# Kernel tuning notes

Hardware: AMD Instinct MI355X
Metric: run time of the kernel (lower is better)

Reference implementation:

```python
import jax, jax.numpy as jnp
import numpy as np

B, C, H, W = 2, 192, 128, 128
DG, K = 4, 9  # deformable groups, kernel taps (3x3)


def conv3x3(x, w, b):
    y = jax.lax.conv_general_dilated(x, w, (1, 1), ((1, 1), (1, 1)),
                                     dimension_numbers=('NCHW', 'OIHW', 'NCHW'))
    return y + b[None, :, None, None]


def deform_sample(x, dy, dx, mask):
    # x: [B,C,H,W]; dy,dx,mask: [B,DG,K,H,W]. Returns [B,C,K,H,W] masked bilinear samples.
    b, c, h, w = x.shape
    cg = c // DG
    kk = jnp.arange(K)
    ky = (kk // 3 - 1).astype(x.dtype)  # kernel row offsets {-1,0,1}, pad=1, stride=1
    kx = (kk % 3 - 1).astype(x.dtype)
    ii = jnp.arange(h, dtype=x.dtype)
    jj = jnp.arange(w, dtype=x.dtype)
    py = ii[None, None, None, :, None] + ky[None, None, :, None, None] + dy  # [B,DG,K,H,W]
    px = jj[None, None, None, None, :] + kx[None, None, :, None, None] + dx
    y0 = jnp.floor(py)
    x0 = jnp.floor(px)
    ly = py - y0
    lx = px - x0
    xf = x.reshape(b, DG, cg, h * w)
    out = jnp.zeros((b, DG, cg, K, h, w), dtype=x.dtype)
    corners = [(y0, x0, (1 - ly) * (1 - lx)), (y0, x0 + 1, (1 - ly) * lx),
               (y0 + 1, x0, ly * (1 - lx)), (y0 + 1, x0 + 1, ly * lx)]
    for yc, xc, wt in corners:
        valid = (yc >= 0) & (yc < h) & (xc >= 0) & (xc < w)  # zero padding outside
        wv = wt * valid.astype(x.dtype)
        idx = (jnp.clip(yc, 0, h - 1) * w + jnp.clip(xc, 0, w - 1)).astype(jnp.int32)
        idxb = jnp.broadcast_to(idx.reshape(b, DG, 1, K * h * w), (b, DG, cg, K * h * w))
        g = jnp.take_along_axis(xf, idxb, axis=3).reshape(b, DG, cg, K, h, w)
        out = out + wv[:, :, None] * g
    out = out * mask[:, :, None]
    return out.reshape(b, c, K, h, w)


def setup_inputs() -> dict:
    key = jax.random.key(0)
    ks = jax.random.split(key, 8)
    f32 = jnp.float32
    x_vq = jax.random.normal(ks[0], (B, C, H, W), f32)
    x_residual = jax.random.normal(ks[1], (B, C, H, W), f32)
    w_off = jax.random.normal(ks[2], (C, 2 * C, 3, 3), f32) * (1.0 / np.sqrt(2 * C * 9))
    b_off = jnp.zeros((C,), f32)
    # conv_offset of DCNv2Pack: C -> 3*DG*K channels; small init keeps offsets moderate
    w_co = jax.random.normal(ks[3], (3 * DG * K, C, 3, 3), f32) * 0.02
    b_co = jnp.zeros((3 * DG * K,), f32)
    w_dcn = jax.random.normal(ks[4], (C, C, 3, 3), f32) * (1.0 / np.sqrt(C * 9))
    b_dcn = jnp.zeros((C,), f32)
    return {"x_vq": x_vq, "x_residual": x_residual, "w_off": w_off, "b_off": b_off,
            "w_co": w_co, "b_co": b_co, "w_dcn": w_dcn, "b_dcn": b_dcn}


def reference(x_vq, x_residual, w_off, b_off, w_co, b_co, w_dcn, b_dcn):
    feat = conv3x3(jnp.concatenate([x_vq, x_residual], axis=1), w_off, b_off)  # [B,C,H,W]
    off_out = conv3x3(feat, w_co, b_co)  # [B,3*DG*K,H,W]
    gk = DG * K
    o1 = off_out[:, :gk]
    o2 = off_out[:, gk:2 * gk]
    mask = jax.nn.sigmoid(off_out[:, 2 * gk:])
    dy = o1.reshape(B, DG, K, H, W)
    dx = o2.reshape(B, DG, K, H, W)
    m = mask.reshape(B, DG, K, H, W)
    sampled = deform_sample(x_vq, dy, dx, m)  # [B,C,K,H,W]
    y = jnp.einsum('ock,bckhw->bohw', w_dcn.reshape(C, C, K), sampled)
    return y + b_dcn[None, :, None, None]
```

## Files before the change

kernel.cpp:

```cpp
#include <hip/hip_runtime.h>
#include <math.h>

#define HH 128
#define WW 128
#define HW 16384
#define BB 2
#define CC 192

typedef __attribute__((ext_vector_type(8)))  short short8;
typedef __attribute__((ext_vector_type(4)))  float f32x4;
typedef __attribute__((ext_vector_type(16))) float f32x16;

static __device__ __forceinline__ short f2bf(float f) {
    unsigned u = __float_as_uint(f);
    unsigned r = (u + 0x7FFFu + ((u >> 16) & 1u)) >> 16;
    return (short)r;
}
static __device__ __forceinline__ float bf2f(short s) {
    return __uint_as_float(((unsigned)(unsigned short)s) << 16);
}

static __device__ __forceinline__ void gl_lds16(const short* gsrc, short* ldst) {
    __builtin_amdgcn_global_load_lds(
        (const __attribute__((address_space(1))) unsigned*)gsrc,
        (__attribute__((address_space(3))) unsigned*)ldst, 16, 0, 0);
}

__global__ __launch_bounds__(256) void to_grp_k(
    const float* __restrict__ xv, const float* __restrict__ xr,
    unsigned short* __restrict__ xg)
{
    const int idx = blockIdx.x * 256 + threadIdx.x;
    const int pos = idx & (HW - 1);
    const int cgb = idx >> 14;
    const int cg  = cgb % 48;
    const int b   = cgb / 48;
    short8 v;
#pragma unroll
    for (int r = 0; r < 8; r++) {
        const int c = cg * 8 + r;
        const float f = (c < 192)
            ? xv[((size_t)(b * 192 + c) << 14) + pos]
            : xr[((size_t)(b * 192 + (c - 192)) << 14) + pos];
        v[r] = f2bf(f);
    }
    *reinterpret_cast<short8*>(xg + (size_t)idx * 8) = v;
}

__global__ void pack_w_k(const float* __restrict__ w, short* __restrict__ wp,
                         int Co, int so, int d1, int s1, int d2, int s2, int s3,
                         int total)
{
    const int idx = blockIdx.x * blockDim.x + threadIdx.x;
    if (idx >= total) return;
    const int lane  = idx & 63;
    const int slot  = (idx >> 6) & 7;
    const int chunk = idx >> 9;
    const int o     = slot * 32 + (lane & 31);
    const int k0    = chunk * 16 + ((lane >> 5) << 3);
    short8 v;
#pragma unroll
    for (int r = 0; r < 8; r++) {
        const int k = k0 + r;
        float f = 0.f;
        if (o < Co) {
            const int rem = k % d1;
            f = w[(size_t)o * so + (k / d1) * s1 + (rem / d2) * s2 + (rem % d2) * s3];
        }
        v[r] = f2bf(f);
    }
    *reinterpret_cast<short8*>(wp + (size_t)idx * 8) = v;
}

template<int MTW, int NC16, bool OUT_GRP>
__global__ __launch_bounds__(256, 2) void conv_g_k(
    const unsigned short* __restrict__ xg,
    const short* __restrict__ wA, const float* __restrict__ bias,
    void* __restrict__ outp, int Cout)
{
    __shared__ __align__(16) short Pbuf[3][2][4096];

    const int t    = threadIdx.x;
    const int lane = t & 63;
    const int wid  = t >> 6;
    const int mg   = wid >> 1;
    const int nt   = wid & 1;
    const int lin  = (blockIdx.z * HH + blockIdx.y) * 2 + blockIdx.x;
    const int og_  = (lin & 7) * 64 + (lin >> 3);
    const int j0   = (og_ & 1) * 64;
    const int i    = (og_ >> 1) & (HH - 1);
    const int b    = og_ >> 8;
    const int px   = j0 + (nt << 5) + (lane & 31);
    const int hi   = lane >> 5;
    constexpr int NQ = NC16 * 9;
    constexpr int NP = NQ / 2;

    const unsigned short* __restrict__ xgb = xg + (size_t)b * (NC16 * 2) * HW * 8;

    f32x16 acc[MTW];
#pragma unroll
    for (int m = 0; m < MTW; m++)
#pragma unroll
        for (int r = 0; r < 16; r++) acc[m][r] = 0.f;

    auto loadB = [&](int qq, short8& dst, bool& vm) {
        const int c16 = qq / 9;
        const int tap = qq - c16 * 9;
        const int iy  = i + tap / 3 - 1;
        const int jx  = px + tap % 3 - 1;
        vm = ((unsigned)iy < HH) && ((unsigned)jx < WW);
        const int iyc = min(max(iy, 0), HH - 1);
        const int jxc = min(max(jx, 0), WW - 1);
        dst = *reinterpret_cast<const short8*>(
            xgb + ((size_t)(c16 * 2 + hi) * HW + (iyc << 7) + jxc) * 8);
    };
    auto stage2 = [&](int chunk, int pb, int sl) {
        gl_lds16(wA + (size_t)chunk * 4096 + t * 8,         &Pbuf[pb][sl][wid * 512]);
        gl_lds16(wA + (size_t)chunk * 4096 + (t + 256) * 8, &Pbuf[pb][sl][2048 + wid * 512]);
    };

    short8 B0, B1, B2, B3, B4, B5;
    bool M0, M1, M2, M3, M4, M5;

    stage2(0, 0, 0); stage2(1, 0, 1);
    loadB(0, B0, M0); loadB(1, B1, M1);
    stage2(2, 1, 0); stage2(3, 1, 1);
    loadB(2, B2, M2); loadB(3, B3, M3);

#define CCHUNK(IBUF, SL, BC, MC)                                              \
    {                                                                         \
        short8 bF = BC;                                                       \
        if (!MC) {                                                            \
            _Pragma("unroll")                                                 \
            for (int r = 0; r < 8; r++) bF[r] = 0;                            \
        }                                                                     \
        const short* ab_ = &Pbuf[IBUF][SL][(mg * MTW) * 512 + lane * 8];      \
        short8 aF[MTW];                                                       \
        _Pragma("unroll")                                                     \
        for (int m = 0; m < MTW; m++)                                         \
            aF[m] = *reinterpret_cast<const short8*>(ab_ + m * 512);          \
        _Pragma("unroll")                                                     \
        for (int m = 0; m < MTW; m++)                                         \
            acc[m] = __builtin_amdgcn_mfma_f32_32x32x16_bf16(aF[m], bF, acc[m], 0, 0, 0); \
    }

#define PSTEP(P, IBUF, SBUF, Bc0, Mc0, Bc1, Mc1, Bn0, Mn0, Bn1, Mn1)          \
    {                                                                         \
        loadB(min(2 * ((P) + 2),     NQ - 1), Bn0, Mn0);                      \
        loadB(min(2 * ((P) + 2) + 1, NQ - 1), Bn1, Mn1);                      \
        asm volatile("s_waitcnt vmcnt(8)" ::: "memory");                      \
        __builtin_amdgcn_s_barrier();                                         \
        __builtin_amdgcn_sched_barrier(0);                                    \
        const int sc0_ = min(2 * ((P) + 2),     NQ - 1);                      \
        const int sc1_ = min(2 * ((P) + 2) + 1, NQ - 1);                      \
        stage2(sc0_, SBUF, 0); stage2(sc1_, SBUF, 1);                         \
        CCHUNK(IBUF, 0, Bc0, Mc0);                                            \
        CCHUNK(IBUF, 1, Bc1, Mc1);                                            \
    }

    for (int pp = 0; pp < NP; pp += 3) {
        PSTEP(pp + 0, 0, 2, B0, M0, B1, M1, B4, M4, B5, M5);
        PSTEP(pp + 1, 1, 0, B2, M2, B3, M3, B0, M0, B1, M1);
        PSTEP(pp + 2, 2, 1, B4, M4, B5, M5, B2, M2, B3, M3);
    }
#undef PSTEP
#undef CCHUNK

    const int pos_o = (i << 7) + px;
    if constexpr (OUT_GRP) {
        unsigned short* fg = (unsigned short*)outp;
#pragma unroll
        for (int m = 0; m < MTW; m++) {
            const int mt32 = mg * MTW + m;
#pragma unroll
            for (int g = 0; g < 4; g++) {
                const int ob = mt32 * 32 + 8 * g + 4 * hi;
                const unsigned s0 = (unsigned short)f2bf(acc[m][4 * g + 0] + bias[ob + 0]);
                const unsigned s1 = (unsigned short)f2bf(acc[m][4 * g + 1] + bias[ob + 1]);
                const unsigned s2 = (unsigned short)f2bf(acc[m][4 * g + 2] + bias[ob + 2]);
                const unsigned s3 = (unsigned short)f2bf(acc[m][4 * g + 3] + bias[ob + 3]);
                const int cg = mt32 * 4 + g;
                *reinterpret_cast<uint2*>(
                    fg + ((size_t)(b * (Cout >> 3) + cg) * HW + pos_o) * 8 + 4 * hi) =
                    make_uint2(s0 | (s1 << 16), s2 | (s3 << 16));
            }
        }
    } else {
        float* of = (float*)outp;
#pragma unroll
        for (int m = 0; m < MTW; m++) {
            const int mt32 = mg * MTW + m;
#pragma unroll
            for (int reg = 0; reg < 16; reg++) {
                const int o = mt32 * 32 + (reg & 3) + ((reg >> 2) << 3) + (hi << 2);
                if (o < Cout)
                    of[((size_t)(b * Cout + o) << 14) + pos_o] = acc[m][reg] + bias[o];
            }
        }
    }
}

__global__ __launch_bounds__(128, 2) void dcn_g_k(
    const unsigned short* __restrict__ xg, const float* __restrict__ off,
    const short* __restrict__ wA, const float* __restrict__ bias,
    float* __restrict__ out)
{
    __shared__ __align__(16) f32x4 eW[1152];
    __shared__ __align__(8)  uint2 eO[1152];

    const int t    = threadIdx.x;
    const int lane = t & 63;
    const int mg   = t >> 6;
    const int lin  = (blockIdx.z * HH + blockIdx.y) * 4 + blockIdx.x;
    const int og_  = (lin & 7) * 128 + (lin >> 3);
    const int jt   = og_ & 3;
    const int i    = (og_ >> 2) & (HH - 1);
    const int b    = og_ >> 9;
    const int j0   = jt * 32;

    for (int e = t; e < 1152; e += 128) {
        const int p  = e & 31;
        const int gk = e >> 5;
        const int kt = gk % 9;
        const int j  = j0 + p;
        const size_t sp = (size_t)b * 108 * HW + (size_t)gk * HW + (i << 7) + j;
        const float dy = off[sp];
        const float dx = off[sp + (size_t)36 * HW];
        const float mv = off[sp + (size_t)72 * HW];
        const float m  = 1.f / (1.f + expf(-mv));
        const float py = (float)(i + kt / 3 - 1) + dy;
        const float px = (float)(j + kt % 3 - 1) + dx;
        const float y0f = floorf(py), x0f = floorf(px);
        const float ly = py - y0f, lx = px - x0f;
        const int y0 = (int)y0f, x0 = (int)x0f;
        const float vy0 = (y0 >= 0 && y0 < HH) ? 1.f : 0.f;
        const float vy1 = (y0 + 1 >= 0 && y0 + 1 < HH) ? 1.f : 0.f;
        const float vx0 = (x0 >= 0 && x0 < WW) ? 1.f : 0.f;
        const float vx1 = (x0 + 1 >= 0 && x0 + 1 < WW) ? 1.f : 0.f;
        f32x4 w4;
        w4[0] = (1.f - ly) * (1.f - lx) * m * vy0 * vx0;
        w4[1] = (1.f - ly) * lx         * m * vy0 * vx1;
        w4[2] = ly         * (1.f - lx) * m * vy1 * vx0;
        w4[3] = ly         * lx         * m * vy1 * vx1;
        const int yc0 = min(max(y0, 0), HH - 1);
        const int yc1 = min(max(y0 + 1, 0), HH - 1);
        const int xc0 = min(max(x0, 0), WW - 1);
        const int xc1 = min(max(x0 + 1, 0), WW - 1);
        eW[e] = w4;
        eO[e] = make_uint2((unsigned)((yc0 << 7) + xc0) | ((unsigned)((yc0 << 7) + xc1) << 16),
                           (unsigned)((yc1 << 7) + xc0) | ((unsigned)((yc1 << 7) + xc1) << 16));
    }
    __syncthreads();

    const int px_l = lane & 31;
    const int hi   = lane >> 5;
    const unsigned short* __restrict__ xgb = xg + (size_t)b * 48 * HW * 8;

    f32x16 acc[3];
#pragma unroll
    for (int m = 0; m < 3; m++)
#pragma unroll
        for (int r = 0; r < 16; r++) acc[m][r] = 0.f;

#define AISSUE(QQ, A0, A1, A2)                                                \
    {                                                                         \
        const int qn_ = min((QQ), 107);                                       \
        const short* ap_ = wA + (size_t)qn_ * 4096 + (mg * 3) * 512 + lane * 8; \
        A0 = *reinterpret_cast<const short8*>(ap_);                           \
        A1 = *reinterpret_cast<const short8*>(ap_ + 512);                     \
        A2 = *reinterpret_cast<const short8*>(ap_ + 1024);                    \
    }

#define GISSUE(QQ, N0, N1, N2, N3, WN)                                        \
    {                                                                         \
        const int qn_   = min((QQ), 107);                                     \
        const int c16n_ = qn_ / 9;                                            \
        const int ktn_  = qn_ - 9 * c16n_;                                    \
        const int e_    = ((c16n_ / 3) * 9 + ktn_) * 32 + px_l;               \
        const uint2 o_  = eO[e_];                                             \
        WN = eW[e_];                                                          \
        const unsigned short* base_ = xgb + (size_t)(c16n_ * 2 + hi) * (HW * 8); \
        N0 = *reinterpret_cast<const short8*>(base_ + (size_t)(o_.x & 0xFFFFu) * 8); \
        N1 = *reinterpret_cast<const short8*>(base_ + (size_t)(o_.x >> 16) * 8);     \
        N2 = *reinterpret_cast<const short8*>(base_ + (size_t)(o_.y & 0xFFFFu) * 8); \
        N3 = *reinterpret_cast<const short8*>(base_ + (size_t)(o_.y >> 16) * 8);     \
    }

#define DSTEP(Q, Ac0, Ac1, Ac2, C0, C1, C2, C3, WC, An0, An1, An2, N0, N1, N2, N3, WN) \
    {                                                                         \
        AISSUE((Q) + 1, An0, An1, An2);                                       \
        GISSUE((Q) + 1, N0, N1, N2, N3, WN);                                  \
        asm volatile("s_waitcnt vmcnt(7)" ::: "memory");                      \
        short8 bF;                                                            \
        _Pragma("unroll")                                                     \
        for (int r = 0; r < 8; r++) {                                         \
            const float v = WC[0] * bf2f(C0[r]) + WC[1] * bf2f(C1[r])         \
                          + WC[2] * bf2f(C2[r]) + WC[3] * bf2f(C3[r]);        \
            bF[r] = f2bf(v);                                                  \
        }                                                                     \
        acc[0] = __builtin_amdgcn_mfma_f32_32x32x16_bf16(Ac0, bF, acc[0], 0, 0, 0); \
        acc[1] = __builtin_amdgcn_mfma_f32_32x32x16_bf16(Ac1, bF, acc[1], 0, 0, 0); \
        acc[2] = __builtin_amdgcn_mfma_f32_32x32x16_bf16(Ac2, bF, acc[2], 0, 0, 0); \
    }

    short8 Aa0, Aa1, Aa2, Ab0, Ab1, Ab2;
    short8 Ga0, Ga1, Ga2, Ga3, Gb0, Gb1, Gb2, Gb3;
    f32x4 wGa, wGb;

    AISSUE(0, Aa0, Aa1, Aa2);
    GISSUE(0, Ga0, Ga1, Ga2, Ga3, wGa);

    for (int q = 0; q < 108; q += 2) {
        DSTEP(q,     Aa0, Aa1, Aa2, Ga0, Ga1, Ga2, Ga3, wGa,
                     Ab0, Ab1, Ab2, Gb0, Gb1, Gb2, Gb3, wGb);
        DSTEP(q + 1, Ab0, Ab1, Ab2, Gb0, Gb1, Gb2, Gb3, wGb,
                     Aa0, Aa1, Aa2, Ga0, Ga1, Ga2, Ga3, wGa);
    }
#undef DSTEP
#undef GISSUE
#undef AISSUE

    const int pos_o = (i << 7) + j0 + px_l;
#pragma unroll
    for (int m = 0; m < 3; m++) {
        const int mt32 = mg * 3 + m;
#pragma unroll
        for (int reg = 0; reg < 16; reg++) {
            const int o = mt32 * 32 + (reg & 3) + ((reg >> 2) << 3) + (hi << 2);
            out[((size_t)(b * CC + o) << 14) + pos_o] = acc[m][reg] + bias[o];
        }
    }
}

extern "C" void kernel_launch(void* const* d_in, const int* in_sizes, int n_in,
                              void* d_out, int out_size, void* d_ws, size_t ws_size,
                              hipStream_t stream)
{
    const float* x_vq  = (const float*)d_in[0];
    const float* x_res = (const float*)d_in[1];
    const float* w_off = (const float*)d_in[2];
    const float* b_off = (const float*)d_in[3];
    const float* w_co  = (const float*)d_in[4];
    const float* b_co  = (const float*)d_in[5];
    const float* w_dcn = (const float*)d_in[6];
    const float* b_dcn = (const float*)d_in[7];
    float* out = (float*)d_out;

    char* ws = (char*)d_ws;
    unsigned short* xg = (unsigned short*)ws;
    const size_t xg_sz = (size_t)BB * 48 * HW * 8 * 2;
    unsigned short* fg = (unsigned short*)(ws + xg_sz);
    const size_t fg_sz = (size_t)BB * 24 * HW * 8 * 2;
    float* offb = (float*)(ws + xg_sz + fg_sz);
    const size_t offb_sz = (size_t)BB * 108 * HW * 4;
    short* wA1 = (short*)(ws + xg_sz + fg_sz + offb_sz);
    short* wA2 = wA1 + (size_t)216 * 4096;
    short* wA3 = wA2 + (size_t)108 * 4096;

    to_grp_k<<<dim3(BB * 48 * HW / 256), 256, 0, stream>>>(x_vq, x_res, xg);

    pack_w_k<<<(216 * 512 + 255) / 256, 256, 0, stream>>>(
        w_off, wA1, 192, 3456, 144, 144, 16, 1, 9, 216 * 512);
    pack_w_k<<<(108 * 512 + 255) / 256, 256, 0, stream>>>(
        w_co, wA2, 108, 1728, 144, 144, 16, 1, 9, 108 * 512);
    pack_w_k<<<(108 * 512 + 255) / 256, 256, 0, stream>>>(
        w_dcn, wA3, 192, 1728, 144, 144, 16, 1, 9, 108 * 512);

    conv_g_k<3, 24, true><<<dim3(2, HH, BB), 256, 0, stream>>>(xg, wA1, b_off, fg, 192);
    conv_g_k<2, 12, false><<<dim3(2, HH, BB), 256, 0, stream>>>(fg, wA2, b_co, offb, 108);
    dcn_g_k<<<dim3(4, HH, BB), 128, 0, stream>>>(xg, offb, wA3, b_dcn, out);
}
```

Baseline: 197.2 us.

## Drop LDS weight staging in conv kernels, deepen DCN gather prefetch, use packed bf16 convert

```diff
diff --git a/kernel.cpp b/kernel.cpp
--- a/kernel.cpp
+++ b/kernel.cpp
@@ -1,4 +1,5 @@
 #include <hip/hip_runtime.h>
+#include <hip/hip_bf16.h>
 #include <math.h>
 
 #define HH 128
@@ -10,20 +11,19 @@
 typedef __attribute__((ext_vector_type(8)))  short short8;
 typedef __attribute__((ext_vector_type(4)))  float f32x4;
 typedef __attribute__((ext_vector_type(16))) float f32x16;
+typedef __attribute__((ext_vector_type(2)))  float f32x2;
+typedef __attribute__((ext_vector_type(4)))  unsigned u32x4;
 
 static __device__ __forceinline__ short f2bf(float f) {
     unsigned u = __float_as_uint(f);
     unsigned r = (u + 0x7FFFu + ((u >> 16) & 1u)) >> 16;
     return (short)r;
 }
-static __device__ __forceinline__ float bf2f(short s) {
-    return __uint_as_float(((unsigned)(unsigned short)s) << 16);
-}
-
-static __device__ __forceinline__ void gl_lds16(const short* gsrc, short* ldst) {
-    __builtin_amdgcn_global_load_lds(
-        (const __attribute__((address_space(1))) unsigned*)gsrc,
-        (__attribute__((address_space(3))) unsigned*)ldst, 16, 0, 0);
+static __device__ __forceinline__ f32x2 unpk(unsigned u) {
+    f32x2 r;
+    r[0] = __uint_as_float(u << 16);
+    r[1] = __uint_as_float(u & 0xFFFF0000u);
+    return r;
 }
 
 __global__ __launch_bounds__(256) void to_grp_k(
@@ -73,27 +73,23 @@
 }
 
 template<int MTW, int NC16, bool OUT_GRP>
-__global__ __launch_bounds__(256, 2) void conv_g_k(
+__global__ __launch_bounds__(128, 2) void conv_g_k(
     const unsigned short* __restrict__ xg,
     const short* __restrict__ wA, const float* __restrict__ bias,
     void* __restrict__ outp, int Cout)
 {
-    __shared__ __align__(16) short Pbuf[3][2][4096];
-
     const int t    = threadIdx.x;
     const int lane = t & 63;
-    const int wid  = t >> 6;
-    const int mg   = wid >> 1;
-    const int nt   = wid & 1;
-    const int lin  = (blockIdx.z * HH + blockIdx.y) * 2 + blockIdx.x;
-    const int og_  = (lin & 7) * 64 + (lin >> 3);
-    const int j0   = (og_ & 1) * 64;
-    const int i    = (og_ >> 1) & (HH - 1);
-    const int b    = og_ >> 8;
-    const int px   = j0 + (nt << 5) + (lane & 31);
+    const int mg   = t >> 6;
+    const int lin  = (blockIdx.z * HH + blockIdx.y) * 4 + blockIdx.x;
+    const int og_  = (lin & 7) * 128 + (lin >> 3);
+    const int jt   = og_ & 3;
+    const int i    = (og_ >> 2) & (HH - 1);
+    const int b    = og_ >> 9;
+    const int j0   = jt * 32;
+    const int px   = j0 + (lane & 31);
     const int hi   = lane >> 5;
     constexpr int NQ = NC16 * 9;
-    constexpr int NP = NQ / 2;
 
     const unsigned short* __restrict__ xgb = xg + (size_t)b * (NC16 * 2) * HW * 8;
 
@@ -103,68 +99,58 @@
 #pragma unroll
         for (int r = 0; r < 16; r++) acc[m][r] = 0.f;
 
-    auto loadB = [&](int qq, short8& dst, bool& vm) {
-        const int c16 = qq / 9;
-        const int tap = qq - c16 * 9;
-        const int iy  = i + tap / 3 - 1;
-        const int jx  = px + tap % 3 - 1;
-        vm = ((unsigned)iy < HH) && ((unsigned)jx < WW);
-        const int iyc = min(max(iy, 0), HH - 1);
-        const int jxc = min(max(jx, 0), WW - 1);
-        dst = *reinterpret_cast<const short8*>(
-            xgb + ((size_t)(c16 * 2 + hi) * HW + (iyc << 7) + jxc) * 8);
-    };
-    auto stage2 = [&](int chunk, int pb, int sl) {
-        gl_lds16(wA + (size_t)chunk * 4096 + t * 8,         &Pbuf[pb][sl][wid * 512]);
-        gl_lds16(wA + (size_t)chunk * 4096 + (t + 256) * 8, &Pbuf[pb][sl][2048 + wid * 512]);
-    };
-
-    short8 B0, B1, B2, B3, B4, B5;
-    bool M0, M1, M2, M3, M4, M5;
-
-    stage2(0, 0, 0); stage2(1, 0, 1);
-    loadB(0, B0, M0); loadB(1, B1, M1);
-    stage2(2, 1, 0); stage2(3, 1, 1);
-    loadB(2, B2, M2); loadB(3, B3, M3);
-
-#define CCHUNK(IBUF, SL, BC, MC)                                              \
-    {                                                                         \
-        short8 bF = BC;                                                       \
-        if (!MC) {                                                            \
+#define LA(QQ, DST)                                                           \
+    {                                                                         \
+        const short* ap_ = wA + (size_t)min((QQ), NQ - 1) * 4096              \
+                              + (mg * MTW) * 512 + lane * 8;                  \
+        _Pragma("unroll")                                                     \
+        for (int m = 0; m < MTW; m++)                                         \
+            DST[m] = *reinterpret_cast<const short8*>(ap_ + m * 512);         \
+    }
+#define LB(QQ, DST, MV)                                                       \
+    {                                                                         \
+        const int qn_  = min((QQ), NQ - 1);                                   \
+        const int c16_ = qn_ / 9;                                             \
+        const int tap_ = qn_ - c16_ * 9;                                      \
+        const int iy_  = i + tap_ / 3 - 1;                                    \
+        const int jx_  = px + tap_ % 3 - 1;                                   \
+        MV = ((unsigned)iy_ < HH) && ((unsigned)jx_ < WW);                    \
+        const int iyc_ = min(max(iy_, 0), HH - 1);                            \
+        const int jxc_ = min(max(jx_, 0), WW - 1);                            \
+        DST = *reinterpret_cast<const short8*>(                               \
+            xgb + ((size_t)(c16_ * 2 + hi) * HW + (iyc_ << 7) + jxc_) * 8);   \
+    }
+
+    short8 As0[MTW], As1[MTW], As2[MTW];
+    short8 Bs0, Bs1, Bs2;
+    bool   Ms0, Ms1, Ms2;
+
+    LA(0, As0); LB(0, Bs0, Ms0);
+    LA(1, As1); LB(1, Bs1, Ms1);
+
+#define CSTEP(Q, Ac, Bc, Mc, An, Bn, Mn)                                      \
+    {                                                                         \
+        LA((Q) + 2, An);                                                      \
+        LB((Q) + 2, Bn, Mn);                                                  \
+        asm volatile("s_waitcnt vmcnt(8)" ::: "memory");                      \
+        short8 bF = Bc;                                                       \
+        if (!Mc) {                                                            \
             _Pragma("unroll")                                                 \
             for (int r = 0; r < 8; r++) bF[r] = 0;                            \
         }                                                                     \
-        const short* ab_ = &Pbuf[IBUF][SL][(mg * MTW) * 512 + lane * 8];      \
-        short8 aF[MTW];                                                       \
         _Pragma("unroll")                                                     \
         for (int m = 0; m < MTW; m++)                                         \
-            aF[m] = *reinterpret_cast<const short8*>(ab_ + m * 512);          \
-        _Pragma("unroll")                                                     \
-        for (int m = 0; m < MTW; m++)                                         \
-            acc[m] = __builtin_amdgcn_mfma_f32_32x32x16_bf16(aF[m], bF, acc[m], 0, 0, 0); \
-    }
-
-#define PSTEP(P, IBUF, SBUF, Bc0, Mc0, Bc1, Mc1, Bn0, Mn0, Bn1, Mn1)          \
-    {                                                                         \
-        loadB(min(2 * ((P) + 2),     NQ - 1), Bn0, Mn0);                      \
-        loadB(min(2 * ((P) + 2) + 1, NQ - 1), Bn1, Mn1);                      \
-        asm volatile("s_waitcnt vmcnt(8)" ::: "memory");                      \
-        __builtin_amdgcn_s_barrier();                                         \
-        __builtin_amdgcn_sched_barrier(0);                                    \
-        const int sc0_ = min(2 * ((P) + 2),     NQ - 1);                      \
-        const int sc1_ = min(2 * ((P) + 2) + 1, NQ - 1);                      \
-        stage2(sc0_, SBUF, 0); stage2(sc1_, SBUF, 1);                         \
-        CCHUNK(IBUF, 0, Bc0, Mc0);                                            \
-        CCHUNK(IBUF, 1, Bc1, Mc1);                                            \
-    }
-
-    for (int pp = 0; pp < NP; pp += 3) {
-        PSTEP(pp + 0, 0, 2, B0, M0, B1, M1, B4, M4, B5, M5);
-        PSTEP(pp + 1, 1, 0, B2, M2, B3, M3, B0, M0, B1, M1);
-        PSTEP(pp + 2, 2, 1, B4, M4, B5, M5, B2, M2, B3, M3);
-    }
-#undef PSTEP
-#undef CCHUNK
+            acc[m] = __builtin_amdgcn_mfma_f32_32x32x16_bf16(Ac[m], bF, acc[m], 0, 0, 0); \
+    }
+
+    for (int q = 0; q < NQ; q += 3) {
+        CSTEP(q,     As0, Bs0, Ms0, As2, Bs2, Ms2);
+        CSTEP(q + 1, As1, Bs1, Ms1, As0, Bs0, Ms0);
+        CSTEP(q + 2, As2, Bs2, Ms2, As1, Bs1, Ms1);
+    }
+#undef CSTEP
+#undef LB
+#undef LA
 
     const int pos_o = (i << 7) + px;
     if constexpr (OUT_GRP) {
@@ -262,13 +248,13 @@
 #pragma unroll
         for (int r = 0; r < 16; r++) acc[m][r] = 0.f;
 
-#define AISSUE(QQ, A0, A1, A2)                                                \
-    {                                                                         \
-        const int qn_ = min((QQ), 107);                                       \
-        const short* ap_ = wA + (size_t)qn_ * 4096 + (mg * 3) * 512 + lane * 8; \
-        A0 = *reinterpret_cast<const short8*>(ap_);                           \
-        A1 = *reinterpret_cast<const short8*>(ap_ + 512);                     \
-        A2 = *reinterpret_cast<const short8*>(ap_ + 1024);                    \
+#define AISSUE(QQ, DST)                                                       \
+    {                                                                         \
+        const short* ap_ = wA + (size_t)min((QQ), 107) * 4096                 \
+                              + (mg * 3) * 512 + lane * 8;                    \
+        DST[0] = *reinterpret_cast<const short8*>(ap_);                       \
+        DST[1] = *reinterpret_cast<const short8*>(ap_ + 512);                 \
+        DST[2] = *reinterpret_cast<const short8*>(ap_ + 1024);                \
     }
 
 #define GISSUE(QQ, N0, N1, N2, N3, WN)                                        \
@@ -280,41 +266,47 @@
         const uint2 o_  = eO[e_];                                             \
         WN = eW[e_];                                                          \
         const unsigned short* base_ = xgb + (size_t)(c16n_ * 2 + hi) * (HW * 8); \
-        N0 = *reinterpret_cast<const short8*>(base_ + (size_t)(o_.x & 0xFFFFu) * 8); \
-        N1 = *reinterpret_cast<const short8*>(base_ + (size_t)(o_.x >> 16) * 8);     \
-        N2 = *reinterpret_cast<const short8*>(base_ + (size_t)(o_.y & 0xFFFFu) * 8); \
-        N3 = *reinterpret_cast<const short8*>(base_ + (size_t)(o_.y >> 16) * 8);     \
-    }
-
-#define DSTEP(Q, Ac0, Ac1, Ac2, C0, C1, C2, C3, WC, An0, An1, An2, N0, N1, N2, N3, WN) \
-    {                                                                         \
-        AISSUE((Q) + 1, An0, An1, An2);                                       \
-        GISSUE((Q) + 1, N0, N1, N2, N3, WN);                                  \
-        asm volatile("s_waitcnt vmcnt(7)" ::: "memory");                      \
-        short8 bF;                                                            \
+        N0 = *reinterpret_cast<const u32x4*>(base_ + (size_t)(o_.x & 0xFFFFu) * 8); \
+        N1 = *reinterpret_cast<const u32x4*>(base_ + (size_t)(o_.x >> 16) * 8);     \
+        N2 = *reinterpret_cast<const u32x4*>(base_ + (size_t)(o_.y & 0xFFFFu) * 8); \
+        N3 = *reinterpret_cast<const u32x4*>(base_ + (size_t)(o_.y >> 16) * 8);     \
+    }
+
+#define DSTEP(Q, Ac, C0, C1, C2, C3, WC, An, N0, N1, N2, N3, WN)              \
+    {                                                                         \
+        AISSUE((Q) + 1, An);                                                  \
+        GISSUE((Q) + 2, N0, N1, N2, N3, WN);                                  \
+        asm volatile("s_waitcnt vmcnt(11)" ::: "memory");                     \
+        u32x4 rv_;                                                            \
         _Pragma("unroll")                                                     \
-        for (int r = 0; r < 8; r++) {                                         \
-            const float v = WC[0] * bf2f(C0[r]) + WC[1] * bf2f(C1[r])         \
-                          + WC[2] * bf2f(C2[r]) + WC[3] * bf2f(C3[r]);        \
-            bF[r] = f2bf(v);                                                  \
+        for (int jj = 0; jj < 4; jj++) {                                      \
+            f32x2 v_ = WC[0] * unpk(C0[jj]) + WC[1] * unpk(C1[jj])            \
+                     + WC[2] * unpk(C2[jj]) + WC[3] * unpk(C3[jj]);           \
+            __hip_bfloat162 h2_ = __float22bfloat162_rn(make_float2(v_[0], v_[1])); \
+            unsigned hu_; __builtin_memcpy(&hu_, &h2_, 4);                    \
+            rv_[jj] = hu_;                                                    \
         }                                                                     \
-        acc[0] = __builtin_amdgcn_mfma_f32_32x32x16_bf16(Ac0, bF, acc[0], 0, 0, 0); \
-        acc[1] = __builtin_amdgcn_mfma_f32_32x32x16_bf16(Ac1, bF, acc[1], 0, 0, 0); \
-        acc[2] = __builtin_amdgcn_mfma_f32_32x32x16_bf16(Ac2, bF, acc[2], 0, 0, 0); \
-    }
-
-    short8 Aa0, Aa1, Aa2, Ab0, Ab1, Ab2;
-    short8 Ga0, Ga1, Ga2, Ga3, Gb0, Gb1, Gb2, Gb3;
-    f32x4 wGa, wGb;
-
-    AISSUE(0, Aa0, Aa1, Aa2);
-    GISSUE(0, Ga0, Ga1, Ga2, Ga3, wGa);
-
-    for (int q = 0; q < 108; q += 2) {
-        DSTEP(q,     Aa0, Aa1, Aa2, Ga0, Ga1, Ga2, Ga3, wGa,
-                     Ab0, Ab1, Ab2, Gb0, Gb1, Gb2, Gb3, wGb);
-        DSTEP(q + 1, Ab0, Ab1, Ab2, Gb0, Gb1, Gb2, Gb3, wGb,
-                     Aa0, Aa1, Aa2, Ga0, Ga1, Ga2, Ga3, wGa);
+        const short8 bF = __builtin_bit_cast(short8, rv_);                    \
+        acc[0] = __builtin_amdgcn_mfma_f32_32x32x16_bf16(Ac[0], bF, acc[0], 0, 0, 0); \
+        acc[1] = __builtin_amdgcn_mfma_f32_32x32x16_bf16(Ac[1], bF, acc[1], 0, 0, 0); \
+        acc[2] = __builtin_amdgcn_mfma_f32_32x32x16_bf16(Ac[2], bF, acc[2], 0, 0, 0); \
+    }
+
+    short8 Aa[3], Ab[3];
+    u32x4 Gx0, Gx1, Gx2, Gx3, Gy0, Gy1, Gy2, Gy3, Gz0, Gz1, Gz2, Gz3;
+    f32x4 wGx, wGy, wGz;
+
+    GISSUE(0, Gx0, Gx1, Gx2, Gx3, wGx);
+    AISSUE(0, Aa);
+    GISSUE(1, Gy0, Gy1, Gy2, Gy3, wGy);
+
+    for (int q = 0; q < 108; q += 6) {
+        DSTEP(q,     Aa, Gx0, Gx1, Gx2, Gx3, wGx, Ab, Gz0, Gz1, Gz2, Gz3, wGz);
+        DSTEP(q + 1, Ab, Gy0, Gy1, Gy2, Gy3, wGy, Aa, Gx0, Gx1, Gx2, Gx3, wGx);
+        DSTEP(q + 2, Aa, Gz0, Gz1, Gz2, Gz3, wGz, Ab, Gy0, Gy1, Gy2, Gy3, wGy);
+        DSTEP(q + 3, Ab, Gx0, Gx1, Gx2, Gx3, wGx, Aa, Gz0, Gz1, Gz2, Gz3, wGz);
+        DSTEP(q + 4, Aa, Gy0, Gy1, Gy2, Gy3, wGy, Ab, Gx0, Gx1, Gx2, Gx3, wGx);
+        DSTEP(q + 5, Ab, Gz0, Gz1, Gz2, Gz3, wGz, Aa, Gy0, Gy1, Gy2, Gy3, wGy);
     }
 #undef DSTEP
 #undef GISSUE
@@ -366,7 +358,8 @@
     pack_w_k<<<(108 * 512 + 255) / 256, 256, 0, stream>>>(
         w_dcn, wA3, 192, 1728, 144, 144, 16, 1, 9, 108 * 512);
 
-    conv_g_k<3, 24, true><<<dim3(2, HH, BB), 256, 0, stream>>>(xg, wA1, b_off, fg, 192);
-    conv_g_k<2, 12, false><<<dim3(2, HH, BB), 256, 0, stream>>>(fg, wA2, b_co, offb, 108);
-    dcn_g_k<<<dim3(4, HH, BB), 128, 0, stream>>>(xg, offb, wA3, b_dcn, out);
-}
+    dim3 grid(4, HH, BB);
+    conv_g_k<3, 24, true><<<grid, 128, 0, stream>>>(xg, wA1, b_off, fg, 192);
+    conv_g_k<2, 12, false><<<grid, 128, 0, stream>>>(fg, wA2, b_co, offb, 108);
+    dcn_g_k<<<grid, 128, 0, stream>>>(xg, offb, wA3, b_dcn, out);
+}
```

After: 204.0 us. 1.03x slower.

## Split bilinear gather across waves and share B fragments through LDS

Applied to the files above, without the earlier changes.

```diff
diff --git a/kernel.cpp b/kernel.cpp
--- a/kernel.cpp
+++ b/kernel.cpp
@@ -1,4 +1,5 @@
 #include <hip/hip_runtime.h>
+#include <hip/hip_bf16.h>
 #include <math.h>
 
 #define HH 128
@@ -10,14 +11,19 @@
 typedef __attribute__((ext_vector_type(8)))  short short8;
 typedef __attribute__((ext_vector_type(4)))  float f32x4;
 typedef __attribute__((ext_vector_type(16))) float f32x16;
+typedef __attribute__((ext_vector_type(2)))  float f32x2;
+typedef __attribute__((ext_vector_type(4)))  unsigned u32x4;
 
 static __device__ __forceinline__ short f2bf(float f) {
     unsigned u = __float_as_uint(f);
     unsigned r = (u + 0x7FFFu + ((u >> 16) & 1u)) >> 16;
     return (short)r;
 }
-static __device__ __forceinline__ float bf2f(short s) {
-    return __uint_as_float(((unsigned)(unsigned short)s) << 16);
+static __device__ __forceinline__ f32x2 unpk(unsigned u) {
+    f32x2 r;
+    r[0] = __uint_as_float(u << 16);
+    r[1] = __uint_as_float(u & 0xFFFF0000u);
+    return r;
 }
 
 static __device__ __forceinline__ void gl_lds16(const short* gsrc, short* ldst) {
@@ -207,10 +213,11 @@
 {
     __shared__ __align__(16) f32x4 eW[1152];
     __shared__ __align__(8)  uint2 eO[1152];
+    __shared__ __align__(16) short bfS[2][2][512];
 
     const int t    = threadIdx.x;
     const int lane = t & 63;
-    const int mg   = t >> 6;
+    const int w    = t >> 6;
     const int lin  = (blockIdx.z * HH + blockIdx.y) * 4 + blockIdx.x;
     const int og_  = (lin & 7) * 128 + (lin >> 3);
     const int jt   = og_ & 3;
@@ -262,15 +269,6 @@
 #pragma unroll
         for (int r = 0; r < 16; r++) acc[m][r] = 0.f;
 
-#define AISSUE(QQ, A0, A1, A2)                                                \
-    {                                                                         \
-        const int qn_ = min((QQ), 107);                                       \
-        const short* ap_ = wA + (size_t)qn_ * 4096 + (mg * 3) * 512 + lane * 8; \
-        A0 = *reinterpret_cast<const short8*>(ap_);                           \
-        A1 = *reinterpret_cast<const short8*>(ap_ + 512);                     \
-        A2 = *reinterpret_cast<const short8*>(ap_ + 1024);                    \
-    }
-
 #define GISSUE(QQ, N0, N1, N2, N3, WN)                                        \
     {                                                                         \
         const int qn_   = min((QQ), 107);                                     \
@@ -280,50 +278,71 @@
         const uint2 o_  = eO[e_];                                             \
         WN = eW[e_];                                                          \
         const unsigned short* base_ = xgb + (size_t)(c16n_ * 2 + hi) * (HW * 8); \
-        N0 = *reinterpret_cast<const short8*>(base_ + (size_t)(o_.x & 0xFFFFu) * 8); \
-        N1 = *reinterpret_cast<const short8*>(base_ + (size_t)(o_.x >> 16) * 8);     \
-        N2 = *reinterpret_cast<const short8*>(base_ + (size_t)(o_.y & 0xFFFFu) * 8); \
-        N3 = *reinterpret_cast<const short8*>(base_ + (size_t)(o_.y >> 16) * 8);     \
-    }
-
-#define DSTEP(Q, Ac0, Ac1, Ac2, C0, C1, C2, C3, WC, An0, An1, An2, N0, N1, N2, N3, WN) \
-    {                                                                         \
-        AISSUE((Q) + 1, An0, An1, An2);                                       \
-        GISSUE((Q) + 1, N0, N1, N2, N3, WN);                                  \
-        asm volatile("s_waitcnt vmcnt(7)" ::: "memory");                      \
-        short8 bF;                                                            \
+        N0 = *reinterpret_cast<const u32x4*>(base_ + (size_t)(o_.x & 0xFFFFu) * 8); \
+        N1 = *reinterpret_cast<const u32x4*>(base_ + (size_t)(o_.x >> 16) * 8);     \
+        N2 = *reinterpret_cast<const u32x4*>(base_ + (size_t)(o_.y & 0xFFFFu) * 8); \
+        N3 = *reinterpret_cast<const u32x4*>(base_ + (size_t)(o_.y >> 16) * 8);     \
+    }
+
+#define AISSUE(PP, DST)                                                       \
+    {                                                                         \
+        const short* a0_ = wA + (size_t)min(2 * (PP),     107) * 4096 + (w * 3) * 512 + lane * 8; \
+        const short* a1_ = wA + (size_t)min(2 * (PP) + 1, 107) * 4096 + (w * 3) * 512 + lane * 8; \
+        DST[0] = *reinterpret_cast<const short8*>(a0_);                       \
+        DST[1] = *reinterpret_cast<const short8*>(a0_ + 512);                 \
+        DST[2] = *reinterpret_cast<const short8*>(a0_ + 1024);                \
+        DST[3] = *reinterpret_cast<const short8*>(a1_);                       \
+        DST[4] = *reinterpret_cast<const short8*>(a1_ + 512);                 \
+        DST[5] = *reinterpret_cast<const short8*>(a1_ + 1024);                \
+    }
+
+#define PAIRSTEP(P, Ac, C0, C1, C2, C3, WC, An, N0, N1, N2, N3, WN)           \
+    {                                                                         \
+        GISSUE(2 * ((P) + 1) + w, N0, N1, N2, N3, WN);                        \
+        AISSUE((P) + 1, An);                                                  \
+        asm volatile("s_waitcnt vmcnt(10)" ::: "memory");                     \
+        u32x4 rv_;                                                            \
         _Pragma("unroll")                                                     \
-        for (int r = 0; r < 8; r++) {                                         \
-            const float v = WC[0] * bf2f(C0[r]) + WC[1] * bf2f(C1[r])         \
-                          + WC[2] * bf2f(C2[r]) + WC[3] * bf2f(C3[r]);        \
-            bF[r] = f2bf(v);                                                  \
+        for (int jj = 0; jj < 4; jj++) {                                      \
+            f32x2 v_ = WC[0] * unpk(C0[jj]) + WC[1] * unpk(C1[jj])            \
+                     + WC[2] * unpk(C2[jj]) + WC[3] * unpk(C3[jj]);           \
+            __hip_bfloat162 h2_ = __float22bfloat162_rn(make_float2(v_[0], v_[1])); \
+            unsigned hu_; __builtin_memcpy(&hu_, &h2_, 4);                    \
+            rv_[jj] = hu_;                                                    \
         }                                                                     \
-        acc[0] = __builtin_amdgcn_mfma_f32_32x32x16_bf16(Ac0, bF, acc[0], 0, 0, 0); \
-        acc[1] = __builtin_amdgcn_mfma_f32_32x32x16_bf16(Ac1, bF, acc[1], 0, 0, 0); \
-        acc[2] = __builtin_amdgcn_mfma_f32_32x32x16_bf16(Ac2, bF, acc[2], 0, 0, 0); \
-    }
-
-    short8 Aa0, Aa1, Aa2, Ab0, Ab1, Ab2;
-    short8 Ga0, Ga1, Ga2, Ga3, Gb0, Gb1, Gb2, Gb3;
-    f32x4 wGa, wGb;
-
-    AISSUE(0, Aa0, Aa1, Aa2);
-    GISSUE(0, Ga0, Ga1, Ga2, Ga3, wGa);
-
-    for (int q = 0; q < 108; q += 2) {
-        DSTEP(q,     Aa0, Aa1, Aa2, Ga0, Ga1, Ga2, Ga3, wGa,
-                     Ab0, Ab1, Ab2, Gb0, Gb1, Gb2, Gb3, wGb);
-        DSTEP(q + 1, Ab0, Ab1, Ab2, Gb0, Gb1, Gb2, Gb3, wGb,
-                     Aa0, Aa1, Aa2, Ga0, Ga1, Ga2, Ga3, wGa);
-    }
-#undef DSTEP
+        *reinterpret_cast<u32x4*>(&bfS[(P) & 1][w][lane * 8]) = rv_;          \
+        asm volatile("s_waitcnt lgkmcnt(0)" ::: "memory");                    \
+        __builtin_amdgcn_s_barrier();                                         \
+        __builtin_amdgcn_sched_barrier(0);                                    \
+        const short8 bf0_ = *reinterpret_cast<const short8*>(&bfS[(P) & 1][0][lane * 8]); \
+        const short8 bf1_ = *reinterpret_cast<const short8*>(&bfS[(P) & 1][1][lane * 8]); \
+        acc[0] = __builtin_amdgcn_mfma_f32_32x32x16_bf16(Ac[0], bf0_, acc[0], 0, 0, 0); \
+        acc[1] = __builtin_amdgcn_mfma_f32_32x32x16_bf16(Ac[1], bf0_, acc[1], 0, 0, 0); \
+        acc[2] = __builtin_amdgcn_mfma_f32_32x32x16_bf16(Ac[2], bf0_, acc[2], 0, 0, 0); \
+        acc[0] = __builtin_amdgcn_mfma_f32_32x32x16_bf16(Ac[3], bf1_, acc[0], 0, 0, 0); \
+        acc[1] = __builtin_amdgcn_mfma_f32_32x32x16_bf16(Ac[4], bf1_, acc[1], 0, 0, 0); \
+        acc[2] = __builtin_amdgcn_mfma_f32_32x32x16_bf16(Ac[5], bf1_, acc[2], 0, 0, 0); \
+    }
+
+    short8 Aa[6], Ab[6];
+    u32x4 Gx0, Gx1, Gx2, Gx3, Gy0, Gy1, Gy2, Gy3;
+    f32x4 wGx, wGy;
+
+    GISSUE(0 + w, Gx0, Gx1, Gx2, Gx3, wGx);
+    AISSUE(0, Aa);
+
+    for (int pr = 0; pr < 54; pr += 2) {
+        PAIRSTEP(pr,     Aa, Gx0, Gx1, Gx2, Gx3, wGx, Ab, Gy0, Gy1, Gy2, Gy3, wGy);
+        PAIRSTEP(pr + 1, Ab, Gy0, Gy1, Gy2, Gy3, wGy, Aa, Gx0, Gx1, Gx2, Gx3, wGx);
+    }
+#undef PAIRSTEP
+#undef AISSUE
 #undef GISSUE
-#undef AISSUE
 
     const int pos_o = (i << 7) + j0 + px_l;
 #pragma unroll
     for (int m = 0; m < 3; m++) {
-        const int mt32 = mg * 3 + m;
+        const int mt32 = w * 3 + m;
 #pragma unroll
         for (int reg = 0; reg < 16; reg++) {
             const int o = mt32 * 32 + (reg & 3) + ((reg >> 2) << 3) + (hi << 2);
```

After: 175.5 us. 1.12x faster.
